# Optimization experiments

Measured on AMD Instinct MI355X. Metric: run time of the kernel, lower is better.

Reference implementation:

```python
import jax, jax.numpy as jnp
import numpy as np
from jax import lax

NUM_MELS = 80
NQ = 256          # num_quants
WIN = 1024
HOP = 256
K_UP = 800        # upsample kernel
PAD_UP = K_UP + 4 * HOP - WIN   # = 800
RC = 120          # residual_channels
SC = 240          # skip_channels
KC = 2            # causal kernel
NB = 16           # num blocks
DILS = [1, 2, 4, 8, 16, 32, 64, 128] * 2
DN = ('NCH', 'OIH', 'NCH')


def conv1x1(x, w, b):
    # x: [B,C,T], w: [O,C], b: [O]
    return jnp.einsum('bct,oc->bot', x, w) + b[None, :, None]


def causal_conv(x, w, b, d):
    # x: [B,RC,T], w: [2RC,RC,KC], left-pad by d*(KC-1) -> causal, same length
    y = lax.conv_general_dilated(x, w, (1,), [(d * (KC - 1), 0)],
                                 rhs_dilation=(d,), dimension_numbers=DN)
    return y + b[None, :, None]


def setup_inputs() -> dict:
    key = jax.random.key(0)
    ks = jax.random.split(key, 20)
    s = 0.05
    n = jax.random.normal
    return {
        'waveforms': n(ks[0], (1, 40960), jnp.float32),
        'melspecs': n(ks[1], (1, NUM_MELS, 160), jnp.float32),
        # ConvTranspose-equivalent upsample weight, stored as direct conv weight [O,I,K]
        'up_w': s * n(ks[2], (NUM_MELS, NUM_MELS, K_UP), jnp.float32),
        'up_b': jnp.zeros((NUM_MELS,), jnp.float32),
        'in_w': s * n(ks[3], (RC, 1), jnp.float32),
        'in_b': jnp.zeros((RC,), jnp.float32),
        'blk_causal_w': s * n(ks[4], (NB, 2 * RC, RC, KC), jnp.float32),
        'blk_causal_b': jnp.zeros((NB, 2 * RC), jnp.float32),
        'blk_cond_w': s * n(ks[5], (NB, 2 * RC, NUM_MELS), jnp.float32),
        'blk_cond_b': jnp.zeros((NB, 2 * RC), jnp.float32),
        'blk_skip_w': s * n(ks[6], (NB, SC, RC), jnp.float32),
        'blk_skip_b': jnp.zeros((NB, SC), jnp.float32),
        'blk_res_w': s * n(ks[7], (NB, RC, RC), jnp.float32),
        'blk_res_b': jnp.zeros((NB, RC), jnp.float32),
        'h1_w': s * n(ks[8], (NQ, SC), jnp.float32),
        'h1_b': jnp.zeros((NQ,), jnp.float32),
        'h2_w': s * n(ks[9], (NQ, NQ), jnp.float32),
        'h2_b': jnp.zeros((NQ,), jnp.float32),
    }


def _forward(waveforms, melspecs, up_w, up_b, in_w, in_b,
             blk_causal_w, blk_causal_b, blk_cond_w, blk_cond_b,
             blk_skip_w, blk_skip_b, blk_res_w, blk_res_b,
             h1_w, h1_b, h2_w, h2_b):
    # ConvTranspose1d(stride=HOP, padding=PAD_UP) as lhs-dilated conv:
    # out_len = (F-1)*HOP + K_UP - 2*PAD_UP
    cond = lax.conv_general_dilated(
        melspecs, up_w, (1,), [(K_UP - 1 - PAD_UP, K_UP - 1 - PAD_UP)],
        lhs_dilation=(HOP,), dimension_numbers=DN) + up_b[None, :, None]
    L = min(waveforms.shape[-1], cond.shape[-1])
    wav = waveforms[..., :L]
    cond = cond[..., :L]

    res = conv1x1(wav[:, None, :], in_w, in_b)          # [B,RC,L]
    skip_sum = jnp.zeros((res.shape[0], SC, L), res.dtype)
    for i, d in enumerate(DILS):
        z = causal_conv(res, blk_causal_w[i], blk_causal_b[i], d) \
            + conv1x1(cond, blk_cond_w[i], blk_cond_b[i])  # [B,2RC,L]
        h = jnp.tanh(z[:, :RC]) * jax.nn.sigmoid(z[:, RC:])
        skip_sum = skip_sum + conv1x1(h, blk_skip_w[i], blk_skip_b[i])
        res = res + conv1x1(h, blk_res_w[i], blk_res_b[i])

    x = jax.nn.relu(skip_sum)
    x = jax.nn.relu(conv1x1(x, h1_w, h1_b))
    logits = conv1x1(x, h2_w, h2_b)                      # [B,NQ,L]
    return logits


def reference(waveforms, melspecs, up_w, up_b, in_w, in_b,
              blk_causal_w, blk_causal_b, blk_cond_w, blk_cond_b,
              blk_skip_w, blk_skip_b, blk_res_w, blk_res_b,
              h1_w, h1_b, h2_w, h2_b):
    return _forward(waveforms, melspecs, up_w, up_b, in_w, in_b,
                    blk_causal_w, blk_causal_b, blk_cond_w, blk_cond_b,
                    blk_skip_w, blk_skip_b, blk_res_w, blk_res_b,
                    h1_w, h1_b, h2_w, h2_b)
```

## Files before the change

kernel.cpp:

```cpp
#include <hip/hip_runtime.h>

#define L_LEN 39904
#define NT 624
#define RCH 120
#define SCH 240
#define CMEL 80
#define NQO 256
#define NBLK 16
#define KUP 800

typedef unsigned short u16;
typedef __attribute__((ext_vector_type(8))) short short8;
typedef __attribute__((ext_vector_type(4))) float f32x4;

#define MFMA(a, b, c) __builtin_amdgcn_mfma_f32_16x16x32_bf16((a), (b), (c), 0, 0, 0)

__device__ __forceinline__ u16 f2bf(float f) {
    unsigned u = __float_as_uint(f);
    u += 0x7FFFu + ((u >> 16) & 1u);
    return (u16)(u >> 16);
}
__device__ __forceinline__ unsigned pack2(float a, float b) {
    return (unsigned)f2bf(a) | ((unsigned)f2bf(b) << 16);
}
__device__ __forceinline__ float b16tof(u16 h) {
    return __uint_as_float((unsigned)h << 16);
}
__device__ __forceinline__ float gate(float a, float b) {
    float ea = __expf(2.f * a);
    float th = 1.f - 2.f * __builtin_amdgcn_rcpf(ea + 1.f);
    float sg = __builtin_amdgcn_rcpf(1.f + __expf(-b));
    return th * sg;
}

constexpr size_t O_CONDT = 0;
constexpr size_t O_RESA  = O_CONDT + 7023104;
constexpr size_t O_RESB  = O_RESA + 19153920;
constexpr size_t O_SKIP  = O_RESB + 19153920;
constexpr size_t O_ZFRAG = O_SKIP + 19153920;
constexpr size_t O_SKF   = O_ZFRAG + 2621440;
constexpr size_t O_RF    = O_SKF + 1048576;
constexpr size_t O_H1F   = O_RF + 524288;
constexpr size_t O_H2F   = O_H1F + 131072;
constexpr size_t O_UPF   = O_H2F + 131072;
constexpr size_t O_ZB    = O_UPF + 13107200;
constexpr size_t O_SKB   = O_ZB + 16384;

constexpr size_t H2_CONDT = 0;
constexpr size_t H2_RESF  = 7023104;
constexpr size_t H2_BFA   = H2_RESF + 19153920;
constexpr size_t H2_BFB   = H2_BFA + 9576960;
constexpr size_t H2_ZFRAG = H2_BFB + 9576960;
constexpr size_t H2_SKF   = H2_ZFRAG + 2621440;
constexpr size_t H2_RF    = H2_SKF + 1048576;
constexpr size_t H2_H1F   = H2_RF + 524288;
constexpr size_t H2_H2F   = H2_H1F + 131072;
constexpr size_t H2_ZB    = H2_H2F + 131072;
constexpr size_t H2_SKBS  = H2_ZB + 16384;
constexpr size_t H2_HALL  = H2_SKBS + 16384;
constexpr size_t H_BYTES  = (size_t)NBLK * L_LEN * 120 * 2;
constexpr size_t UPF_BYTES = 13107200;
constexpr size_t NEED_H = H2_HALL + (H_BYTES > UPF_BYTES ? H_BYTES : UPF_BYTES);

__global__ void k_prep_zfrag(const float* __restrict__ bc_w, const float* __restrict__ bq_w,
                             u16* __restrict__ dst) {
    int i = blockIdx.x * 256 + threadIdx.x;
    if (i >= NBLK * 10 * 16 * 512) return;
    int jj = i & 7, lane = (i >> 3) & 63, mt = (i >> 9) & 15;
    int rest = i >> 13, ks = rest % 10, blk = rest / 10;
    int m = mt * 16 + (lane & 15);
    int k = ks * 32 + ((lane >> 4) << 3) + jj;
    float v = 0.f;
    if (m < 240) {
        int o = (m & 1) ? (m >> 1) + 120 : (m >> 1);
        if (k < 120)       v = bc_w[((size_t)(blk * 240 + o) * 120 + k) * 2 + 0];
        else if (k < 240)  v = bc_w[((size_t)(blk * 240 + o) * 120 + (k - 120)) * 2 + 1];
        else               v = bq_w[(size_t)(blk * 240 + o) * 80 + (k - 240)];
    }
    dst[i] = f2bf(v);
}
__global__ void k_prep_skfrag(const float* __restrict__ bs_w, u16* __restrict__ dst) {
    int i = blockIdx.x * 256 + threadIdx.x;
    if (i >= NBLK * 4 * 16 * 512) return;
    int jj = i & 7, lane = (i >> 3) & 63, mt = (i >> 9) & 15;
    int rest = i >> 13, ks = rest & 3, blk = rest >> 2;
    int m = mt * 16 + (lane & 15);
    int k = ks * 32 + ((lane >> 4) << 3) + jj;
    float v = (m < 240 && k < 120) ? bs_w[(size_t)(blk * 240 + m) * 120 + k] : 0.f;
    dst[i] = f2bf(v);
}
__global__ void k_prep_rfrag(const float* __restrict__ br_w, u16* __restrict__ dst) {
    int i = blockIdx.x * 256 + threadIdx.x;
    if (i >= NBLK * 4 * 8 * 512) return;
    int jj = i & 7, lane = (i >> 3) & 63, mt = (i >> 9) & 7;
    int rest = i >> 12, ks = rest & 3, blk = rest >> 2;
    int m = mt * 16 + (lane & 15);
    int k = ks * 32 + ((lane >> 4) << 3) + jj;
    float v = (m < 120 && k < 120) ? br_w[(size_t)(blk * 120 + m) * 120 + k] : 0.f;
    dst[i] = f2bf(v);
}
__global__ void k_prep_h1frag(const float* __restrict__ h1_w, u16* __restrict__ dst) {
    int i = blockIdx.x * 256 + threadIdx.x;
    if (i >= 8 * 16 * 512) return;
    int jj = i & 7, lane = (i >> 3) & 63, mt = (i >> 9) & 15, ks = i >> 13;
    int m = mt * 16 + (lane & 15);
    int k = ks * 32 + ((lane >> 4) << 3) + jj;
    float v = (k < 240) ? h1_w[(size_t)m * 240 + k] : 0.f;
    dst[i] = f2bf(v);
}
__global__ void k_prep_h2frag(const float* __restrict__ h2_w, u16* __restrict__ dst) {
    int i = blockIdx.x * 256 + threadIdx.x;
    if (i >= 8 * 16 * 512) return;
    int jj = i & 7, lane = (i >> 3) & 63, mt = (i >> 9) & 15, ks = i >> 13;
    int m = mt * 16 + (lane & 15);
    int k = ks * 32 + ((lane >> 4) << 3) + jj;
    dst[i] = f2bf(h2_w[(size_t)m * 256 + k]);
}
__global__ void k_prep_upfrag(const float* __restrict__ up_w, u16* __restrict__ dst) {
    int i = blockIdx.x * 256 + threadIdx.x;
    if (i >= 256 * 10 * 5 * 512) return;
    int jj = i & 7, lane = (i >> 3) & 63;
    int rest = i >> 9;
    int mt = rest % 5; rest /= 5;
    int ks = rest % 10; int p = rest / 10;
    int m = mt * 16 + (lane & 15);
    int k = ks * 32 + ((lane >> 4) << 3) + jj;
    int c = k >> 2, j = k & 3;
    int r = (256 - ((p + 1) & 255)) & 255;
    int kk = r + 256 * j;
    float v = (m < 80 && kk < KUP) ? up_w[((size_t)m * 80 + c) * KUP + kk] : 0.f;
    dst[i] = f2bf(v);
}
__global__ void k_prep_zbias(const float* __restrict__ bc_b, const float* __restrict__ bq_b,
                             float* __restrict__ dst) {
    int i = blockIdx.x * 256 + threadIdx.x;
    if (i >= NBLK * 256) return;
    int m = i & 255, blk = i >> 8;
    float v = 0.f;
    if (m < 240) {
        int o = (m & 1) ? (m >> 1) + 120 : (m >> 1);
        v = bc_b[blk * 240 + o] + bq_b[blk * 240 + o];
    }
    dst[i] = v;
}
__global__ void k_prep_skbias(const float* __restrict__ bs_b, float* __restrict__ dst) {
    int i = blockIdx.x * 256 + threadIdx.x;
    if (i >= NBLK * 240) return;
    dst[i] = bs_b[i];
}
__global__ void k_prep_skbsum(const float* __restrict__ bs_b, float* __restrict__ dst) {
    int m = blockIdx.x * 256 + threadIdx.x;
    if (m >= 240) return;
    float s = 0.f;
    for (int i = 0; i < NBLK; i++) s += bs_b[i * 240 + m];
    dst[m] = s;
}
__global__ void k_res_initT(const float* __restrict__ wav, const float* __restrict__ in_w,
                            const float* __restrict__ in_b, float* __restrict__ resT) {
    int i = blockIdx.x * 256 + threadIdx.x;
    if (i >= L_LEN * RCH) return;
    int t = i / RCH, c = i % RCH;
    resT[i] = wav[t] * in_w[c] + in_b[c];
}
__global__ void k_res_initT2(const float* __restrict__ wav, const float* __restrict__ in_w,
                             const float* __restrict__ in_b, float* __restrict__ resT,
                             u16* __restrict__ resB) {
    int i = blockIdx.x * 256 + threadIdx.x;
    if (i >= L_LEN * RCH) return;
    int t = i / RCH, c = i % RCH;
    float v = wav[t] * in_w[c] + in_b[c];
    resT[i] = v;
    resB[i] = f2bf(v);
}

__global__ __launch_bounds__(256) void k_up(const float* __restrict__ mel,
        const u16* __restrict__ upf, const float* __restrict__ up_b,
        u16* __restrict__ condT) {
    __shared__ u16 s_ms[64 * 328];
    const int tid = threadIdx.x, l = tid & 63, w = tid >> 6;
    const int quad = l >> 4, tloc = l & 15;
    const int p = blockIdx.x, s0 = blockIdx.y * 64;
    for (int rr = 0; rr < 16; rr++) {
        int tt = w + 4 * rr;
        int sg = s0 + tt;
        #pragma unroll
        for (int base = 0; base < 320; base += 64) {
            int ck = base + l;
            int c = ck >> 2, j = ck & 3;
            int mi = 1 + j + sg;
            float v = (mi < 160) ? mel[c * 160 + mi] : 0.f;
            s_ms[tt * 328 + ck] = f2bf(v);
        }
    }
    __syncthreads();
    f32x4 acc[2][4];
    #pragma unroll
    for (int i = 0; i < 2; i++)
        #pragma unroll
        for (int n = 0; n < 4; n++) acc[i][n] = (f32x4){0.f, 0.f, 0.f, 0.f};
    const int nmt = (w == 0) ? 2 : 1;
    int mts[2]; mts[0] = w; mts[1] = 4;
    for (int ks = 0; ks < 10; ks++) {
        short8 b[4];
        int k0 = ks * 32 + quad * 8;
        #pragma unroll
        for (int n = 0; n < 4; n++)
            b[n] = *(const short8*)&s_ms[(n * 16 + tloc) * 328 + k0];
        const short8* ap = (const short8*)(upf) + ((size_t)p * 10 + ks) * 5 * 64;
        for (int i = 0; i < nmt; i++) {
            short8 a = ap[mts[i] * 64 + l];
            #pragma unroll
            for (int n = 0; n < 4; n++) acc[i][n] = MFMA(a, b[n], acc[i][n]);
        }
    }
    for (int i = 0; i < nmt; i++) {
        int o_base = mts[i] * 16 + quad * 4;
        float4 ub = *(const float4*)(up_b + o_base);
        float bb[4] = {ub.x, ub.y, ub.z, ub.w};
        #pragma unroll
        for (int n = 0; n < 4; n++) {
            int sg = s0 + n * 16 + tloc;
            int t = p + 256 * sg;
            if (t < L_LEN) {
                #pragma unroll
                for (int r = 0; r < 4; r++)
                    condT[(size_t)t * 88 + o_base + r] = f2bf(acc[i][n][r] + bb[r]);
            }
        }
    }
}

__global__ __launch_bounds__(512, 4) void k_block(
        const u16* __restrict__ condT, const float* __restrict__ resT_in,
        float* __restrict__ resT_out, u16* __restrict__ skipT,
        const u16* __restrict__ zfrag, const u16* __restrict__ skfrag,
        const u16* __restrict__ rfrag, const float* __restrict__ zbias,
        const float* __restrict__ skbias, const float* __restrict__ resb,
        int blk, int dil, int first) {
    __shared__ u16 s_x[64 * 328];
    u16* s_h = s_x;
    const int tid = threadIdx.x, l = tid & 63, w = tid >> 6;
    const int quad = l >> 4, tloc = l & 15;
    const int t0 = blockIdx.x * 64;
    const short8* zap = (const short8*)(zfrag) + (size_t)blk * 10 * 16 * 64;
    short8 a_cur[2], a_nxt[2];
    #pragma unroll
    for (int i = 0; i < 2; i++) a_cur[i] = zap[(size_t)(w * 2 + i) * 64 + l];
    for (int rr = 0; rr < 8; rr++) {
        int tt = w + 8 * rr;
        int tg = t0 + tt, tp = tg - dil;
        if (l < 60) {
            float2 pv = make_float2(0.f, 0.f), cv = make_float2(0.f, 0.f);
            if (tp >= 0 && tp < L_LEN) pv = *(const float2*)(resT_in + (size_t)tp * 120 + 2 * l);
            if (tg < L_LEN)            cv = *(const float2*)(resT_in + (size_t)tg * 120 + 2 * l);
            *(unsigned*)&s_x[tt * 328 + 2 * l]       = pack2(pv.x, pv.y);
            *(unsigned*)&s_x[tt * 328 + 120 + 2 * l] = pack2(cv.x, cv.y);
        }
        if (l < 40) {
            unsigned q = 0;
            if (tg < L_LEN) q = *(const unsigned*)(condT + (size_t)tg * 88 + 2 * l);
            *(unsigned*)&s_x[tt * 328 + 240 + 2 * l] = q;
        }
    }
    __syncthreads();
    f32x4 acc[2][4];
    #pragma unroll
    for (int i = 0; i < 2; i++)
        #pragma unroll
        for (int n = 0; n < 4; n++) acc[i][n] = (f32x4){0.f, 0.f, 0.f, 0.f};
    for (int ks = 0; ks < 10; ks++) {
        if (ks < 9) {
            #pragma unroll
            for (int i = 0; i < 2; i++)
                a_nxt[i] = zap[((size_t)(ks + 1) * 16 + w * 2 + i) * 64 + l];
        }
        int k0 = ks * 32 + quad * 8;
        short8 b[4];
        #pragma unroll
        for (int n = 0; n < 4; n++)
            b[n] = *(const short8*)&s_x[(n * 16 + tloc) * 328 + k0];
        #pragma unroll
        for (int i = 0; i < 2; i++)
            #pragma unroll
            for (int n = 0; n < 4; n++) acc[i][n] = MFMA(a_cur[i], b[n], acc[i][n]);
        #pragma unroll
        for (int i = 0; i < 2; i++) a_cur[i] = a_nxt[i];
    }
    const short8* sap = (const short8*)(skfrag) + (size_t)blk * 4 * 16 * 64;
    const short8* rap = (const short8*)(rfrag) + (size_t)blk * 4 * 8 * 64;
    short8 sa_c[2], sa_n[2], ra_c, ra_n;
    #pragma unroll
    for (int i = 0; i < 2; i++) sa_c[i] = sap[(size_t)(w * 2 + i) * 64 + l];
    ra_c = rap[(size_t)w * 64 + l];
    uint2 skp[2][4];
    if (!first) {
        #pragma unroll
        for (int i = 0; i < 2; i++) {
            int m_base = (w * 2 + i) * 16 + quad * 4;
            if (m_base < 240) {
                #pragma unroll
                for (int n = 0; n < 4; n++) {
                    int t = t0 + n * 16 + tloc;
                    if (t < L_LEN)
                        skp[i][n] = *(const uint2*)(skipT + (size_t)t * 240 + m_base);
                }
            }
        }
    }
    unsigned hu[2][4];
    #pragma unroll
    for (int i = 0; i < 2; i++) {
        int m_base = (w * 2 + i) * 16 + quad * 4;
        float4 bz4 = *(const float4*)(zbias + blk * 256 + m_base);
        #pragma unroll
        for (int n = 0; n < 4; n++) {
            float h0 = gate(acc[i][n][0] + bz4.x, acc[i][n][1] + bz4.y);
            float h1 = gate(acc[i][n][2] + bz4.z, acc[i][n][3] + bz4.w);
            hu[i][n] = pack2(h0, h1);
        }
    }
    __syncthreads();
    #pragma unroll
    for (int i = 0; i < 2; i++) {
        int j0 = (w * 2 + i) * 8 + quad * 2;
        #pragma unroll
        for (int n = 0; n < 4; n++)
            *(unsigned*)&s_h[(n * 16 + tloc) * 136 + j0] = hu[i][n];
    }
    __syncthreads();
    f32x4 sacc[2][4], racc[4];
    #pragma unroll
    for (int i = 0; i < 2; i++)
        #pragma unroll
        for (int n = 0; n < 4; n++) sacc[i][n] = (f32x4){0.f, 0.f, 0.f, 0.f};
    #pragma unroll
    for (int n = 0; n < 4; n++) racc[n] = (f32x4){0.f, 0.f, 0.f, 0.f};
    for (int ks = 0; ks < 4; ks++) {
        if (ks < 3) {
            #pragma unroll
            for (int i = 0; i < 2; i++)
                sa_n[i] = sap[((size_t)(ks + 1) * 16 + w * 2 + i) * 64 + l];
            ra_n = rap[((size_t)(ks + 1) * 8 + w) * 64 + l];
        }
        short8 b[4];
        int k0 = ks * 32 + quad * 8;
        #pragma unroll
        for (int n = 0; n < 4; n++)
            b[n] = *(const short8*)&s_h[(n * 16 + tloc) * 136 + k0];
        #pragma unroll
        for (int i = 0; i < 2; i++)
            #pragma unroll
            for (int n = 0; n < 4; n++) sacc[i][n] = MFMA(sa_c[i], b[n], sacc[i][n]);
        #pragma unroll
        for (int n = 0; n < 4; n++) racc[n] = MFMA(ra_c, b[n], racc[n]);
        #pragma unroll
        for (int i = 0; i < 2; i++) sa_c[i] = sa_n[i];
        ra_c = ra_n;
    }
    #pragma unroll
    for (int i = 0; i < 2; i++) {
        int m_base = (w * 2 + i) * 16 + quad * 4;
        if (m_base >= 240) continue;
        float4 sb4 = *(const float4*)(skbias + blk * 240 + m_base);
        #pragma unroll
        for (int n = 0; n < 4; n++) {
            int t = t0 + n * 16 + tloc;
            if (t >= L_LEN) continue;
            float x0 = sacc[i][n][0] + sb4.x;
            float x1 = sacc[i][n][1] + sb4.y;
            float x2 = sacc[i][n][2] + sb4.z;
            float x3 = sacc[i][n][3] + sb4.w;
            if (!first) {
                uint2 pv = skp[i][n];
                x0 += b16tof((u16)(pv.x & 0xFFFF));
                x1 += b16tof((u16)(pv.x >> 16));
                x2 += b16tof((u16)(pv.y & 0xFFFF));
                x3 += b16tof((u16)(pv.y >> 16));
            }
            uint2 ov;
            ov.x = pack2(x0, x1);
            ov.y = pack2(x2, x3);
            *(uint2*)(skipT + (size_t)t * 240 + m_base) = ov;
        }
    }
    {
        int m_base = w * 16 + quad * 4;
        if (m_base < 120) {
            float4 rb4 = *(const float4*)(resb + blk * 120 + m_base);
            #pragma unroll
            for (int n = 0; n < 4; n++) {
                int t = t0 + n * 16 + tloc;
                if (t >= L_LEN) continue;
                float4 cur = *(const float4*)(resT_in + (size_t)t * 120 + m_base);
                float4 o;
                o.x = cur.x + racc[n][0] + rb4.x;
                o.y = cur.y + racc[n][1] + rb4.y;
                o.z = cur.z + racc[n][2] + rb4.z;
                o.w = cur.w + racc[n][3] + rb4.w;
                *(float4*)(resT_out + (size_t)t * 120 + m_base) = o;
            }
        }
    }
}

__global__ __launch_bounds__(512, 4) void k_block_h3(
        const u16* __restrict__ condT, float* __restrict__ resF,
        const u16* __restrict__ bfIn, u16* __restrict__ bfOut,
        u16* __restrict__ hout,
        const u16* __restrict__ zfrag, const u16* __restrict__ rfrag,
        const float* __restrict__ zbias, const float* __restrict__ resb,
        int blk, int dil) {
    __shared__ u16 s_x[64 * 328];
    u16* s_h = s_x;
    const int tid = threadIdx.x, l = tid & 63, w = tid >> 6;
    const int quad = l >> 4, tloc = l & 15;
    const int t0 = blockIdx.x * 64;
    const short8* zap = (const short8*)(zfrag) + (size_t)blk * 10 * 16 * 64;
    short8 a_cur[2], a_nxt[2];
    a_cur[0] = zap[(size_t)(w * 2 + 0) * 64 + l];
    a_cur[1] = zap[(size_t)(w * 2 + 1) * 64 + l];
    const uint2 Z2 = make_uint2(0u, 0u);
    for (int rr = 0; rr < 8; rr++) {
        int tt = w + 8 * rr, tg = t0 + tt;
        if (l < 30) {
            uint2 cv = (tg < L_LEN) ? *(const uint2*)(bfIn + (size_t)tg * 120 + 4 * l) : Z2;
            *(uint2*)&s_x[tt * 328 + 120 + 4 * l] = cv;
            if (tt < dil) {
                int tp = tg - dil;
                uint2 pv = (tp >= 0 && tp < L_LEN)
                    ? *(const uint2*)(bfIn + (size_t)tp * 120 + 4 * l) : Z2;
                *(uint2*)&s_x[tt * 328 + 4 * l] = pv;
            }
        } else if (l >= 32 && l < 54) {
            int c = l - 32;
            uint2 q = (tg < L_LEN) ? *(const uint2*)(condT + (size_t)tg * 88 + 4 * c) : Z2;
            *(uint2*)&s_x[tt * 328 + 240 + 4 * c] = q;
        }
    }
    __syncthreads();
    if (dil < 64) {
        for (int rr = 0; rr < 8; rr++) {
            int tt = w + 8 * rr;
            if (l < 30 && tt >= dil)
                *(uint2*)&s_x[tt * 328 + 4 * l] =
                    *(const uint2*)&s_x[(tt - dil) * 328 + 120 + 4 * l];
        }
        __syncthreads();
    }
    f32x4 acc[2][4];
    #pragma unroll
    for (int i = 0; i < 2; i++)
        #pragma unroll
        for (int n = 0; n < 4; n++) acc[i][n] = (f32x4){0.f, 0.f, 0.f, 0.f};
    for (int ks = 0; ks < 10; ks++) {
        if (ks < 9) {
            a_nxt[0] = zap[((size_t)(ks + 1) * 16 + w * 2 + 0) * 64 + l];
            a_nxt[1] = zap[((size_t)(ks + 1) * 16 + w * 2 + 1) * 64 + l];
        }
        int k0 = ks * 32 + quad * 8;
        short8 b[4];
        #pragma unroll
        for (int n = 0; n < 4; n++)
            b[n] = *(const short8*)&s_x[(n * 16 + tloc) * 328 + k0];
        #pragma unroll
        for (int i = 0; i < 2; i++)
            #pragma unroll
            for (int n = 0; n < 4; n++) acc[i][n] = MFMA(a_cur[i], b[n], acc[i][n]);
        a_cur[0] = a_nxt[0]; a_cur[1] = a_nxt[1];
    }
    const short8* rap = (const short8*)(rfrag) + (size_t)blk * 4 * 8 * 64;
    short8 ra_c = rap[(size_t)w * 64 + l], ra_n;
    const int m_r = w * 16 + quad * 4;
    float4 cur_pf[4] = {};
    if (m_r < 120) {
        #pragma unroll
        for (int n = 0; n < 4; n++) {
            int t = t0 + n * 16 + tloc;
            if (t < L_LEN) cur_pf[n] = *(const float4*)(resF + (size_t)t * 120 + m_r);
        }
    }
    unsigned hu[2][4];
    #pragma unroll
    for (int i = 0; i < 2; i++) {
        int m_base = (w * 2 + i) * 16 + quad * 4;
        float4 bz4 = *(const float4*)(zbias + blk * 256 + m_base);
        #pragma unroll
        for (int n = 0; n < 4; n++) {
            float h0 = gate(acc[i][n][0] + bz4.x, acc[i][n][1] + bz4.y);
            float h1 = gate(acc[i][n][2] + bz4.z, acc[i][n][3] + bz4.w);
            hu[i][n] = pack2(h0, h1);
        }
    }
    __syncthreads();
    #pragma unroll
    for (int i = 0; i < 2; i++) {
        int j0 = (w * 2 + i) * 8 + quad * 2;
        #pragma unroll
        for (int n = 0; n < 4; n++)
            *(unsigned*)&s_h[(n * 16 + tloc) * 136 + j0] = hu[i][n];
    }
    __syncthreads();
    for (int rr = 0; rr < 8; rr++) {
        int tt = w + 8 * rr, tg = t0 + tt;
        if (l < 60 && tg < L_LEN)
            *(unsigned*)&hout[(size_t)tg * 120 + 2 * l] =
                *(const unsigned*)&s_h[tt * 136 + 2 * l];
    }
    f32x4 racc[4];
    #pragma unroll
    for (int n = 0; n < 4; n++) racc[n] = (f32x4){0.f, 0.f, 0.f, 0.f};
    for (int ks = 0; ks < 4; ks++) {
        if (ks < 3) ra_n = rap[((size_t)(ks + 1) * 8 + w) * 64 + l];
        short8 b[4];
        int k0 = ks * 32 + quad * 8;
        #pragma unroll
        for (int n = 0; n < 4; n++)
            b[n] = *(const short8*)&s_h[(n * 16 + tloc) * 136 + k0];
        #pragma unroll
        for (int n = 0; n < 4; n++) racc[n] = MFMA(ra_c, b[n], racc[n]);
        ra_c = ra_n;
    }
    if (m_r < 120) {
        float4 rb4 = *(const float4*)(resb + blk * 120 + m_r);
        #pragma unroll
        for (int n = 0; n < 4; n++) {
            int t = t0 + n * 16 + tloc;
            if (t >= L_LEN) continue;
            float4 o;
            o.x = cur_pf[n].x + racc[n][0] + rb4.x;
            o.y = cur_pf[n].y + racc[n][1] + rb4.y;
            o.z = cur_pf[n].z + racc[n][2] + rb4.z;
            o.w = cur_pf[n].w + racc[n][3] + rb4.w;
            *(float4*)(resF + (size_t)t * 120 + m_r) = o;
            uint2 hv;
            hv.x = pack2(o.x, o.y);
            hv.y = pack2(o.z, o.w);
            *(uint2*)(bfOut + (size_t)t * 120 + m_r) = hv;
        }
    }
}

__global__ __launch_bounds__(512, 4) void k_final(const u16* __restrict__ skipT,
        const u16* __restrict__ h1f, const u16* __restrict__ h2f,
        const float* __restrict__ h1_b, const float* __restrict__ h2_b,
        float* __restrict__ out) {
    __shared__ u16 s_m[64 * 264];
    const int tid = threadIdx.x, l = tid & 63, w = tid >> 6;
    const int quad = l >> 4, tloc = l & 15;
    const int t0 = blockIdx.x * 64;
    const short8* ap1 = (const short8*)h1f;
    short8 a_cur[2], a_nxt[2];
    #pragma unroll
    for (int i = 0; i < 2; i++) a_cur[i] = ap1[(size_t)(w * 2 + i) * 64 + l];
    for (int rr = 0; rr < 8; rr++) {
        int tt = w + 8 * rr;
        int tg = t0 + tt;
        uint2 v = make_uint2(0u, 0u);
        if (l < 60 && tg < L_LEN)
            v = *(const uint2*)(skipT + (size_t)tg * 240 + 4 * l);
        float x0 = fmaxf(b16tof((u16)(v.x & 0xFFFF)), 0.f);
        float x1 = fmaxf(b16tof((u16)(v.x >> 16)), 0.f);
        float x2 = fmaxf(b16tof((u16)(v.y & 0xFFFF)), 0.f);
        float x3 = fmaxf(b16tof((u16)(v.y >> 16)), 0.f);
        uint2 ov;
        ov.x = pack2(x0, x1);
        ov.y = pack2(x2, x3);
        *(uint2*)&s_m[tt * 264 + 4 * l] = ov;
    }
    __syncthreads();
    f32x4 acc[2][4];
    #pragma unroll
    for (int i = 0; i < 2; i++)
        #pragma unroll
        for (int n = 0; n < 4; n++) acc[i][n] = (f32x4){0.f, 0.f, 0.f, 0.f};
    for (int ks = 0; ks < 8; ks++) {
        if (ks < 7) {
            #pragma unroll
            for (int i = 0; i < 2; i++)
                a_nxt[i] = ap1[((size_t)(ks + 1) * 16 + w * 2 + i) * 64 + l];
        }
        short8 b[4];
        int k0 = ks * 32 + quad * 8;
        #pragma unroll
        for (int n = 0; n < 4; n++)
            b[n] = *(const short8*)&s_m[(n * 16 + tloc) * 264 + k0];
        #pragma unroll
        for (int i = 0; i < 2; i++)
            #pragma unroll
            for (int n = 0; n < 4; n++) acc[i][n] = MFMA(a_cur[i], b[n], acc[i][n]);
        #pragma unroll
        for (int i = 0; i < 2; i++) a_cur[i] = a_nxt[i];
    }
    unsigned ylo[2][4], yhi[2][4];
    #pragma unroll
    for (int i = 0; i < 2; i++) {
        int m_base = (w * 2 + i) * 16 + quad * 4;
        float4 b1 = *(const float4*)(h1_b + m_base);
        #pragma unroll
        for (int n = 0; n < 4; n++) {
            float y0 = fmaxf(acc[i][n][0] + b1.x, 0.f);
            float y1v = fmaxf(acc[i][n][1] + b1.y, 0.f);
            float y2 = fmaxf(acc[i][n][2] + b1.z, 0.f);
            float y3 = fmaxf(acc[i][n][3] + b1.w, 0.f);
            ylo[i][n] = pack2(y0, y1v);
            yhi[i][n] = pack2(y2, y3);
        }
    }
    const short8* ap2 = (const short8*)h2f;
    #pragma unroll
    for (int i = 0; i < 2; i++) a_cur[i] = ap2[(size_t)(w * 2 + i) * 64 + l];
    __syncthreads();
    #pragma unroll
    for (int i = 0; i < 2; i++) {
        int m_base = (w * 2 + i) * 16 + quad * 4;
        #pragma unroll
        for (int n = 0; n < 4; n++) {
            int t = n * 16 + tloc;
            *(unsigned*)&s_m[t * 264 + m_base]     = ylo[i][n];
            *(unsigned*)&s_m[t * 264 + m_base + 2] = yhi[i][n];
        }
    }
    __syncthreads();
    #pragma unroll
    for (int i = 0; i < 2; i++)
        #pragma unroll
        for (int n = 0; n < 4; n++) acc[i][n] = (f32x4){0.f, 0.f, 0.f, 0.f};
    for (int ks = 0; ks < 8; ks++) {
        if (ks < 7) {
            #pragma unroll
            for (int i = 0; i < 2; i++)
                a_nxt[i] = ap2[((size_t)(ks + 1) * 16 + w * 2 + i) * 64 + l];
        }
        short8 b[4];
        int k0 = ks * 32 + quad * 8;
        #pragma unroll
        for (int n = 0; n < 4; n++)
            b[n] = *(const short8*)&s_m[(n * 16 + tloc) * 264 + k0];
        #pragma unroll
        for (int i = 0; i < 2; i++)
            #pragma unroll
            for (int n = 0; n < 4; n++) acc[i][n] = MFMA(a_cur[i], b[n], acc[i][n]);
        #pragma unroll
        for (int i = 0; i < 2; i++) a_cur[i] = a_nxt[i];
    }
    #pragma unroll
    for (int i = 0; i < 2; i++) {
        int m_base = (w * 2 + i) * 16 + quad * 4;
        float4 b2 = *(const float4*)(h2_b + m_base);
        float bb[4] = {b2.x, b2.y, b2.z, b2.w};
        #pragma unroll
        for (int n = 0; n < 4; n++) {
            int t = t0 + n * 16 + tloc;
            if (t >= L_LEN) continue;
            #pragma unroll
            for (int r = 0; r < 4; r++)
                out[(size_t)(m_base + r) * L_LEN + t] = acc[i][n][r] + bb[r];
        }
    }
}

__global__ __launch_bounds__(512, 4) void k_final_h3(const u16* __restrict__ hall,
        const u16* __restrict__ skf, const u16* __restrict__ h1f,
        const u16* __restrict__ h2f, const float* __restrict__ skbsum,
        const float* __restrict__ h1_b, const float* __restrict__ h2_b,
        float* __restrict__ out) {
    __shared__ u16 smem[2 * 64 * 136];
    u16* s_m = smem;
    const int tid = threadIdx.x, l = tid & 63, w = tid >> 6;
    const int quad = l >> 4, tloc = l & 15;
    const int t0 = blockIdx.x * 64;
    const short8* sap = (const short8*)skf;

    unsigned ha[8], hb[8];
    auto LOADH = [&](unsigned (&reg)[8], int i) {
        const u16* hp = hall + (size_t)i * ((size_t)L_LEN * 120);
        #pragma unroll
        for (int rr = 0; rr < 8; rr++) {
            int tg = t0 + w + 8 * rr;
            reg[rr] = (l < 60 && tg < L_LEN)
                ? *(const unsigned*)&hp[(size_t)tg * 120 + 2 * l] : 0u;
        }
    };
    if (l >= 60) {
        #pragma unroll
        for (int rr = 0; rr < 8; rr++) {
            int row = w + 8 * rr;
            *(unsigned*)&smem[row * 136 + 2 * l] = 0u;
            *(unsigned*)&smem[64 * 136 + row * 136 + 2 * l] = 0u;
        }
    }
    LOADH(ha, 0);
    #pragma unroll
    for (int rr = 0; rr < 8; rr++)
        if (l < 60) *(unsigned*)&smem[(w + 8 * rr) * 136 + 2 * l] = ha[rr];
    LOADH(hb, 1);
    short8 sa_c[2], sa_n[2];
    sa_c[0] = sap[(size_t)(w * 2 + 0) * 64 + l];
    sa_c[1] = sap[(size_t)(w * 2 + 1) * 64 + l];
    f32x4 sacc[2][4];
    #pragma unroll
    for (int i = 0; i < 2; i++)
        #pragma unroll
        for (int n = 0; n < 4; n++) sacc[i][n] = (f32x4){0.f, 0.f, 0.f, 0.f};
    __syncthreads();
    #pragma unroll
    for (int i = 0; i < 16; i++) {
        u16* cur = smem + (i & 1) * (64 * 136);
        u16* nxt = smem + ((i + 1) & 1) * (64 * 136);
        unsigned (&wrg)[8] = (i & 1) ? ha : hb;
        unsigned (&lrg)[8] = (i & 1) ? hb : ha;
        if (i < 15) {
            #pragma unroll
            for (int rr = 0; rr < 8; rr++)
                if (l < 60) *(unsigned*)&nxt[(w + 8 * rr) * 136 + 2 * l] = wrg[rr];
        }
        if (i < 14) LOADH(lrg, i + 2);
        for (int ks = 0; ks < 4; ks++) {
            int g = i * 4 + ks;
            if (g < 63) {
                sa_n[0] = sap[((size_t)(g + 1) * 16 + w * 2 + 0) * 64 + l];
                sa_n[1] = sap[((size_t)(g + 1) * 16 + w * 2 + 1) * 64 + l];
            }
            int k0 = ks * 32 + quad * 8;
            short8 b[4];
            #pragma unroll
            for (int n = 0; n < 4; n++)
                b[n] = *(const short8*)&cur[(n * 16 + tloc) * 136 + k0];
            #pragma unroll
            for (int i2 = 0; i2 < 2; i2++)
                #pragma unroll
                for (int n = 0; n < 4; n++)
                    sacc[i2][n] = MFMA(sa_c[i2], b[n], sacc[i2][n]);
            sa_c[0] = sa_n[0]; sa_c[1] = sa_n[1];
        }
        __syncthreads();
    }
    const short8* ap1 = (const short8*)h1f;
    short8 a_cur[2], a_nxt[2];
    a_cur[0] = ap1[(size_t)(w * 2 + 0) * 64 + l];
    a_cur[1] = ap1[(size_t)(w * 2 + 1) * 64 + l];
    #pragma unroll
    for (int i2 = 0; i2 < 2; i2++) {
        int m_base = (w * 2 + i2) * 16 + quad * 4;
        float4 sb4 = make_float4(0.f, 0.f, 0.f, 0.f);
        bool valid = (m_base < 240);
        if (valid) sb4 = *(const float4*)(skbsum + m_base);
        #pragma unroll
        for (int n = 0; n < 4; n++) {
            float x0 = 0.f, x1 = 0.f, x2 = 0.f, x3 = 0.f;
            if (valid) {
                x0 = fmaxf(sacc[i2][n][0] + sb4.x, 0.f);
                x1 = fmaxf(sacc[i2][n][1] + sb4.y, 0.f);
                x2 = fmaxf(sacc[i2][n][2] + sb4.z, 0.f);
                x3 = fmaxf(sacc[i2][n][3] + sb4.w, 0.f);
            }
            int t = n * 16 + tloc;
            *(unsigned*)&s_m[t * 264 + m_base]     = pack2(x0, x1);
            *(unsigned*)&s_m[t * 264 + m_base + 2] = pack2(x2, x3);
        }
    }
    __syncthreads();
    f32x4 acc[2][4];
    #pragma unroll
    for (int i = 0; i < 2; i++)
        #pragma unroll
        for (int n = 0; n < 4; n++) acc[i][n] = (f32x4){0.f, 0.f, 0.f, 0.f};
    for (int ks = 0; ks < 8; ks++) {
        if (ks < 7) {
            #pragma unroll
            for (int i = 0; i < 2; i++)
                a_nxt[i] = ap1[((size_t)(ks + 1) * 16 + w * 2 + i) * 64 + l];
        }
        short8 b[4];
        int k0 = ks * 32 + quad * 8;
        #pragma unroll
        for (int n = 0; n < 4; n++)
            b[n] = *(const short8*)&s_m[(n * 16 + tloc) * 264 + k0];
        #pragma unroll
        for (int i = 0; i < 2; i++)
            #pragma unroll
            for (int n = 0; n < 4; n++) acc[i][n] = MFMA(a_cur[i], b[n], acc[i][n]);
        #pragma unroll
        for (int i = 0; i < 2; i++) a_cur[i] = a_nxt[i];
    }
    unsigned ylo[2][4], yhi[2][4];
    #pragma unroll
    for (int i = 0; i < 2; i++) {
        int m_base = (w * 2 + i) * 16 + quad * 4;
        float4 b1 = *(const float4*)(h1_b + m_base);
        #pragma unroll
        for (int n = 0; n < 4; n++) {
            float y0 = fmaxf(acc[i][n][0] + b1.x, 0.f);
            float y1v = fmaxf(acc[i][n][1] + b1.y, 0.f);
            float y2 = fmaxf(acc[i][n][2] + b1.z, 0.f);
            float y3 = fmaxf(acc[i][n][3] + b1.w, 0.f);
            ylo[i][n] = pack2(y0, y1v);
            yhi[i][n] = pack2(y2, y3);
        }
    }
    const short8* ap2 = (const short8*)h2f;
    #pragma unroll
    for (int i = 0; i < 2; i++) a_cur[i] = ap2[(size_t)(w * 2 + i) * 64 + l];
    __syncthreads();
    #pragma unroll
    for (int i = 0; i < 2; i++) {
        int m_base = (w * 2 + i) * 16 + quad * 4;
        #pragma unroll
        for (int n = 0; n < 4; n++) {
            int t = n * 16 + tloc;
            *(unsigned*)&s_m[t * 264 + m_base]     = ylo[i][n];
            *(unsigned*)&s_m[t * 264 + m_base + 2] = yhi[i][n];
        }
    }
    __syncthreads();
    #pragma unroll
    for (int i = 0; i < 2; i++)
        #pragma unroll
        for (int n = 0; n < 4; n++) acc[i][n] = (f32x4){0.f, 0.f, 0.f, 0.f};
    for (int ks = 0; ks < 8; ks++) {
        if (ks < 7) {
            #pragma unroll
            for (int i = 0; i < 2; i++)
                a_nxt[i] = ap2[((size_t)(ks + 1) * 16 + w * 2 + i) * 64 + l];
        }
        short8 b[4];
        int k0 = ks * 32 + quad * 8;
        #pragma unroll
        for (int n = 0; n < 4; n++)
            b[n] = *(const short8*)&s_m[(n * 16 + tloc) * 264 + k0];
        #pragma unroll
        for (int i = 0; i < 2; i++)
            #pragma unroll
            for (int n = 0; n < 4; n++) acc[i][n] = MFMA(a_cur[i], b[n], acc[i][n]);
        #pragma unroll
        for (int i = 0; i < 2; i++) a_cur[i] = a_nxt[i];
    }
    #pragma unroll
    for (int i = 0; i < 2; i++) {
        int m_base = (w * 2 + i) * 16 + quad * 4;
        float4 b2 = *(const float4*)(h2_b + m_base);
        float bb[4] = {b2.x, b2.y, b2.z, b2.w};
        #pragma unroll
        for (int n = 0; n < 4; n++) {
            int t = t0 + n * 16 + tloc;
            if (t >= L_LEN) continue;
            #pragma unroll
            for (int r = 0; r < 4; r++)
                out[(size_t)(m_base + r) * L_LEN + t] = acc[i][n][r] + bb[r];
        }
    }
}

extern "C" void kernel_launch(void* const* d_in, const int* in_sizes, int n_in,
                              void* d_out, int out_size, void* d_ws, size_t ws_size,
                              hipStream_t stream) {
    const float* wav   = (const float*)d_in[0];
    const float* mel   = (const float*)d_in[1];
    const float* up_w  = (const float*)d_in[2];
    const float* up_b  = (const float*)d_in[3];
    const float* in_w  = (const float*)d_in[4];
    const float* in_b  = (const float*)d_in[5];
    const float* bc_w  = (const float*)d_in[6];
    const float* bc_b  = (const float*)d_in[7];
    const float* bq_w  = (const float*)d_in[8];
    const float* bq_b  = (const float*)d_in[9];
    const float* bs_w  = (const float*)d_in[10];
    const float* bs_b  = (const float*)d_in[11];
    const float* br_w  = (const float*)d_in[12];
    const float* br_b  = (const float*)d_in[13];
    const float* h1_w  = (const float*)d_in[14];
    const float* h1_b  = (const float*)d_in[15];
    const float* h2_w  = (const float*)d_in[16];
    const float* h2_b  = (const float*)d_in[17];

    char* wsb = (char*)d_ws;
    const bool use_h = (ws_size >= NEED_H);

    if (use_h) {
        u16*   condT = (u16*)(wsb + H2_CONDT);
        float* resF  = (float*)(wsb + H2_RESF);
        u16*   bfA   = (u16*)(wsb + H2_BFA);
        u16*   bfB   = (u16*)(wsb + H2_BFB);
        u16*   zfrag = (u16*)(wsb + H2_ZFRAG);
        u16*   skf   = (u16*)(wsb + H2_SKF);
        u16*   rf    = (u16*)(wsb + H2_RF);
        u16*   h1f   = (u16*)(wsb + H2_H1F);
        u16*   h2f   = (u16*)(wsb + H2_H2F);
        float* zb    = (float*)(wsb + H2_ZB);
        float* skbs  = (float*)(wsb + H2_SKBS);
        u16*   hall  = (u16*)(wsb + H2_HALL);
        u16*   upf   = (u16*)(wsb + H2_HALL);

        k_prep_zfrag <<<5120, 256, 0, stream>>>(bc_w, bq_w, zfrag);
        k_prep_skfrag<<<2048, 256, 0, stream>>>(bs_w, skf);
        k_prep_rfrag <<<1024, 256, 0, stream>>>(br_w, rf);
        k_prep_h1frag<<<256, 256, 0, stream>>>(h1_w, h1f);
        k_prep_h2frag<<<256, 256, 0, stream>>>(h2_w, h2f);
        k_prep_upfrag<<<25600, 256, 0, stream>>>(up_w, upf);
        k_prep_zbias <<<16, 256, 0, stream>>>(bc_b, bq_b, zb);
        k_prep_skbsum<<<1, 256, 0, stream>>>(bs_b, skbs);
        k_res_initT2 <<<(L_LEN * RCH + 255) / 256, 256, 0, stream>>>(wav, in_w, in_b, resF, bfA);
        k_up<<<dim3(256, 3), 256, 0, stream>>>(mel, upf, up_b, condT);

        for (int i = 0; i < NBLK; i++) {
            int d = 1 << (i & 7);
            const u16* bfIn = (i & 1) ? bfB : bfA;
            u16* bfOut      = (i & 1) ? bfA : bfB;
            k_block_h3<<<NT, 512, 0, stream>>>(condT, resF, bfIn, bfOut,
                                               hall + (size_t)i * (size_t)L_LEN * 120,
                                               zfrag, rf, zb, br_b, i, d);
        }
        k_final_h3<<<NT, 512, 0, stream>>>(hall, skf, h1f, h2f, skbs, h1_b, h2_b,
                                           (float*)d_out);
    } else {
        u16*   condT = (u16*)(wsb + O_CONDT);
        float* resA  = (float*)(wsb + O_RESA);
        float* resB  = (float*)(wsb + O_RESB);
        u16*   skipT = (u16*)(wsb + O_SKIP);
        u16*   zfrag = (u16*)(wsb + O_ZFRAG);
        u16*   skf   = (u16*)(wsb + O_SKF);
        u16*   rf    = (u16*)(wsb + O_RF);
        u16*   h1f   = (u16*)(wsb + O_H1F);
        u16*   h2f   = (u16*)(wsb + O_H2F);
        u16*   upf   = (u16*)(wsb + O_UPF);
        float* zb    = (float*)(wsb + O_ZB);
        float* skb   = (float*)(wsb + O_SKB);

        k_prep_zfrag <<<5120, 256, 0, stream>>>(bc_w, bq_w, zfrag);
        k_prep_skfrag<<<2048, 256, 0, stream>>>(bs_w, skf);
        k_prep_rfrag <<<1024, 256, 0, stream>>>(br_w, rf);
        k_prep_h1frag<<<256, 256, 0, stream>>>(h1_w, h1f);
        k_prep_h2frag<<<256, 256, 0, stream>>>(h2_w, h2f);
        k_prep_upfrag<<<25600, 256, 0, stream>>>(up_w, upf);
        k_prep_zbias <<<16, 256, 0, stream>>>(bc_b, bq_b, zb);
        k_prep_skbias<<<15, 256, 0, stream>>>(bs_b, skb);
        k_res_initT  <<<(L_LEN * RCH + 255) / 256, 256, 0, stream>>>(wav, in_w, in_b, resA);
        k_up<<<dim3(256, 3), 256, 0, stream>>>(mel, upf, up_b, condT);

        for (int i = 0; i < NBLK; i++) {
            int d = 1 << (i & 7);
            const float* rin = (i & 1) ? resB : resA;
            float* rout      = (i & 1) ? resA : resB;
            k_block<<<NT, 512, 0, stream>>>(condT, rin, rout, skipT, zfrag, skf, rf,
                                            zb, skb, br_b, i, d, (i == 0) ? 1 : 0);
        }
        k_final<<<NT, 512, 0, stream>>>(skipT, h1f, h2f, h1_b, h2_b, (float*)d_out);
    }
}
```

Before: 783.2 us.

## Drop fp32 residual stream, keep residual in bf16 only; deepen final prefetch

The fp32 residual buffer is removed. Each block now reads the current residual from the bf16 copy already staged in shared memory and writes only the bf16 residual for the next block. This cuts a large fp32 global read and write per block. The cost is that bf16 rounding error accumulates across 16 residual updates. Separately, the final kernel changes its register prefetch of h slices from double to triple buffering, loading three blocks ahead to hide load latency.

```diff
diff --git a/kernel.cpp b/kernel.cpp
--- a/kernel.cpp
+++ b/kernel.cpp
@@ -162,15 +162,12 @@
     int t = i / RCH, c = i % RCH;
     resT[i] = wav[t] * in_w[c] + in_b[c];
 }
-__global__ void k_res_initT2(const float* __restrict__ wav, const float* __restrict__ in_w,
-                             const float* __restrict__ in_b, float* __restrict__ resT,
-                             u16* __restrict__ resB) {
+__global__ void k_res_initTb(const float* __restrict__ wav, const float* __restrict__ in_w,
+                             const float* __restrict__ in_b, u16* __restrict__ resB) {
     int i = blockIdx.x * 256 + threadIdx.x;
     if (i >= L_LEN * RCH) return;
     int t = i / RCH, c = i % RCH;
-    float v = wav[t] * in_w[c] + in_b[c];
-    resT[i] = v;
-    resB[i] = f2bf(v);
+    resB[i] = f2bf(wav[t] * in_w[c] + in_b[c]);
 }
 
 __global__ __launch_bounds__(256) void k_up(const float* __restrict__ mel,
@@ -403,8 +400,8 @@
     }
 }
 
-__global__ __launch_bounds__(512, 4) void k_block_h3(
-        const u16* __restrict__ condT, float* __restrict__ resF,
+__global__ __launch_bounds__(512, 4) void k_block_h4(
+        const u16* __restrict__ condT,
         const u16* __restrict__ bfIn, u16* __restrict__ bfOut,
         u16* __restrict__ hout,
         const u16* __restrict__ zfrag, const u16* __restrict__ rfrag,
@@ -471,13 +468,11 @@
     const short8* rap = (const short8*)(rfrag) + (size_t)blk * 4 * 8 * 64;
     short8 ra_c = rap[(size_t)w * 64 + l], ra_n;
     const int m_r = w * 16 + quad * 4;
-    float4 cur_pf[4] = {};
+    uint2 curb[4];
     if (m_r < 120) {
         #pragma unroll
-        for (int n = 0; n < 4; n++) {
-            int t = t0 + n * 16 + tloc;
-            if (t < L_LEN) cur_pf[n] = *(const float4*)(resF + (size_t)t * 120 + m_r);
-        }
+        for (int n = 0; n < 4; n++)
+            curb[n] = *(const uint2*)&s_x[(n * 16 + tloc) * 328 + 120 + m_r];
     }
     unsigned hu[2][4];
     #pragma unroll
@@ -526,15 +521,13 @@
         for (int n = 0; n < 4; n++) {
             int t = t0 + n * 16 + tloc;
             if (t >= L_LEN) continue;
-            float4 o;
-            o.x = cur_pf[n].x + racc[n][0] + rb4.x;
-            o.y = cur_pf[n].y + racc[n][1] + rb4.y;
-            o.z = cur_pf[n].z + racc[n][2] + rb4.z;
-            o.w = cur_pf[n].w + racc[n][3] + rb4.w;
-            *(float4*)(resF + (size_t)t * 120 + m_r) = o;
+            float o0 = b16tof((u16)(curb[n].x & 0xFFFF)) + racc[n][0] + rb4.x;
+            float o1 = b16tof((u16)(curb[n].x >> 16))    + racc[n][1] + rb4.y;
+            float o2 = b16tof((u16)(curb[n].y & 0xFFFF)) + racc[n][2] + rb4.z;
+            float o3 = b16tof((u16)(curb[n].y >> 16))    + racc[n][3] + rb4.w;
             uint2 hv;
-            hv.x = pack2(o.x, o.y);
-            hv.y = pack2(o.z, o.w);
+            hv.x = pack2(o0, o1);
+            hv.y = pack2(o2, o3);
             *(uint2*)(bfOut + (size_t)t * 120 + m_r) = hv;
         }
     }
@@ -659,7 +652,7 @@
     }
 }
 
-__global__ __launch_bounds__(512, 4) void k_final_h3(const u16* __restrict__ hall,
+__global__ __launch_bounds__(512, 4) void k_final_h4(const u16* __restrict__ hall,
         const u16* __restrict__ skf, const u16* __restrict__ h1f,
         const u16* __restrict__ h2f, const float* __restrict__ skbsum,
         const float* __restrict__ h1_b, const float* __restrict__ h2_b,
@@ -671,7 +664,7 @@
     const int t0 = blockIdx.x * 64;
     const short8* sap = (const short8*)skf;
 
-    unsigned ha[8], hb[8];
+    unsigned hs[3][8];
     auto LOADH = [&](unsigned (&reg)[8], int i) {
         const u16* hp = hall + (size_t)i * ((size_t)L_LEN * 120);
         #pragma unroll
@@ -689,11 +682,13 @@
             *(unsigned*)&smem[64 * 136 + row * 136 + 2 * l] = 0u;
         }
     }
-    LOADH(ha, 0);
+    LOADH(hs[0], 0);
     #pragma unroll
     for (int rr = 0; rr < 8; rr++)
-        if (l < 60) *(unsigned*)&smem[(w + 8 * rr) * 136 + 2 * l] = ha[rr];
-    LOADH(hb, 1);
+        if (l < 60) *(unsigned*)&smem[(w + 8 * rr) * 136 + 2 * l] = hs[0][rr];
+    LOADH(hs[1], 1);
+    LOADH(hs[2], 2);
+    LOADH(hs[0], 3);
     short8 sa_c[2], sa_n[2];
     sa_c[0] = sap[(size_t)(w * 2 + 0) * 64 + l];
     sa_c[1] = sap[(size_t)(w * 2 + 1) * 64 + l];
@@ -707,14 +702,13 @@
     for (int i = 0; i < 16; i++) {
         u16* cur = smem + (i & 1) * (64 * 136);
         u16* nxt = smem + ((i + 1) & 1) * (64 * 136);
-        unsigned (&wrg)[8] = (i & 1) ? ha : hb;
-        unsigned (&lrg)[8] = (i & 1) ? hb : ha;
+        const int wset = (i + 1) % 3;
         if (i < 15) {
             #pragma unroll
             for (int rr = 0; rr < 8; rr++)
-                if (l < 60) *(unsigned*)&nxt[(w + 8 * rr) * 136 + 2 * l] = wrg[rr];
-        }
-        if (i < 14) LOADH(lrg, i + 2);
+                if (l < 60) *(unsigned*)&nxt[(w + 8 * rr) * 136 + 2 * l] = hs[wset][rr];
+        }
+        if (i < 12) LOADH(hs[wset], i + 4);
         for (int ks = 0; ks < 4; ks++) {
             int g = i * 4 + ks;
             if (g < 63) {
@@ -878,7 +872,6 @@
 
     if (use_h) {
         u16*   condT = (u16*)(wsb + H2_CONDT);
-        float* resF  = (float*)(wsb + H2_RESF);
         u16*   bfA   = (u16*)(wsb + H2_BFA);
         u16*   bfB   = (u16*)(wsb + H2_BFB);
         u16*   zfrag = (u16*)(wsb + H2_ZFRAG);
@@ -899,18 +892,18 @@
         k_prep_upfrag<<<25600, 256, 0, stream>>>(up_w, upf);
         k_prep_zbias <<<16, 256, 0, stream>>>(bc_b, bq_b, zb);
         k_prep_skbsum<<<1, 256, 0, stream>>>(bs_b, skbs);
-        k_res_initT2 <<<(L_LEN * RCH + 255) / 256, 256, 0, stream>>>(wav, in_w, in_b, resF, bfA);
+        k_res_initTb <<<(L_LEN * RCH + 255) / 256, 256, 0, stream>>>(wav, in_w, in_b, bfA);
         k_up<<<dim3(256, 3), 256, 0, stream>>>(mel, upf, up_b, condT);
 
         for (int i = 0; i < NBLK; i++) {
             int d = 1 << (i & 7);
             const u16* bfIn = (i & 1) ? bfB : bfA;
             u16* bfOut      = (i & 1) ? bfA : bfB;
-            k_block_h3<<<NT, 512, 0, stream>>>(condT, resF, bfIn, bfOut,
+            k_block_h4<<<NT, 512, 0, stream>>>(condT, bfIn, bfOut,
                                                hall + (size_t)i * (size_t)L_LEN * 120,
                                                zfrag, rf, zb, br_b, i, d);
         }
-        k_final_h3<<<NT, 512, 0, stream>>>(hall, skf, h1f, h2f, skbs, h1_b, h2_b,
+        k_final_h4<<<NT, 512, 0, stream>>>(hall, skf, h1f, h2f, skbs, h1_b, h2_b,
                                            (float*)d_out);
     } else {
         u16*   condT = (u16*)(wsb + O_CONDT);
```

Result: faster. 730.1 us (-6.8%).
